# Kernel tuning notes

Measured on AMD Instinct MI355X. Metric: run time of the kernel, lower is better.

The kernel has to match this reference:

```python
import jax, jax.numpy as jnp
import numpy as np

NUM_HEADS = 16
D_MODEL = 1024


def setup_inputs() -> dict:
    key = jax.random.key(0)
    k1, k2, k3 = jax.random.split(key, 3)
    x = jax.random.normal(k1, (4, 2048, D_MODEL), dtype=jnp.float32)
    # torch.nn.Linear weights are [out_features, in_features]
    w_qkv = jax.random.normal(k2, (3 * D_MODEL, D_MODEL), dtype=jnp.float32) * (1.0 / np.sqrt(D_MODEL))
    w_o = jax.random.normal(k3, (D_MODEL, D_MODEL), dtype=jnp.float32) * (1.0 / np.sqrt(D_MODEL))
    return {"x": x, "w_qkv": w_qkv, "w_o": w_o}


def reference(x, w_qkv, w_o):
    b, n, _ = x.shape
    h = NUM_HEADS
    dh = D_MODEL // h  # head dim
    qkv = jnp.einsum('bnd,ed->bne', x, w_qkv)            # (b, n, 3*d_model)
    # Faithful to: rearrange(qkv, 'b n (h d) -> b h n d', h=h) then chunk(3, dim=-1)
    qkv = qkv.reshape(b, n, h, 3 * dh).transpose(0, 2, 1, 3)  # (b, h, n, 3*dh)
    q, k, v = jnp.split(qkv, 3, axis=-1)                 # each (b, h, n, dh)
    scale = 1.0 / jnp.sqrt(jnp.asarray(dh, dtype=x.dtype))
    scores = jnp.einsum('bhqd,bhkd->bhqk', q, k) * scale  # (b, h, n, n)
    attn = jax.nn.softmax(scores, axis=-1)
    out = jnp.einsum('bhqk,bhkd->bhqd', attn, v)          # (b, h, n, dh)
    out = out.transpose(0, 2, 1, 3).reshape(b, n, h * dh)  # 'b h n d -> b n (h d)'
    return jnp.einsum('bnd,ed->bne', out, w_o)
```

## Files before the change

kernel.cpp:

```cpp
#include <hip/hip_runtime.h>

#define BATCH 4
#define SEQ 2048
#define DM 1024
#define NH 16
#define DH 64
#define M_TOT (BATCH * SEQ)
#define EQKV (3 * DM)
#define QSCALE 0.18033688011112042f

typedef __bf16 bf16x8 __attribute__((ext_vector_type(8)));
typedef unsigned short u16x8 __attribute__((ext_vector_type(8)));
typedef float f32x2 __attribute__((ext_vector_type(2)));
typedef float f32x4 __attribute__((ext_vector_type(4)));
typedef float f32x16 __attribute__((ext_vector_type(16)));

static __device__ __forceinline__ unsigned short f2bf(float f) {
    unsigned int u = __builtin_bit_cast(unsigned int, f);
    u += 0x7fffu + ((u >> 16) & 1u);
    return (unsigned short)(u >> 16);
}

static __device__ __forceinline__ unsigned short f2bf_fast(float f) {
    return (unsigned short)((__builtin_bit_cast(unsigned int, f) + 0x8000u) >> 16);
}

static __device__ __forceinline__ unsigned int cvt_pk_bf16(float lo, float hi) {
    unsigned int r;
    asm("v_cvt_pk_bf16_f32 %0, %1, %2" : "=v"(r) : "v"(lo), "v"(hi));
    return r;
}

static __device__ __forceinline__ f32x2 pk_add(f32x2 a, f32x2 b) {
    f32x2 d;
    asm("v_pk_add_f32 %0, %1, %2" : "=v"(d) : "v"(a), "v"(b));
    return d;
}

static __device__ __forceinline__ float fast_exp2(float x) {
#if __has_builtin(__builtin_amdgcn_exp2f)
    return __builtin_amdgcn_exp2f(x);
#else
    return exp2f(x);
#endif
}

static __device__ __forceinline__ bf16x8 ld_frag(const ushort* p) {
    return *(const bf16x8*)p;
}

static __device__ __forceinline__ bf16x8 mk_frag(unsigned int a, unsigned int b,
                                                 unsigned int c, unsigned int d) {
    union { unsigned int u[4]; bf16x8 v; } t;
    t.u[0] = a; t.u[1] = b; t.u[2] = c; t.u[3] = d;
    return t.v;
}

static __device__ __forceinline__ void gload_lds16(const ushort* g, ushort* l) {
    __builtin_amdgcn_global_load_lds(
        (const __attribute__((address_space(1))) unsigned int*)g,
        (__attribute__((address_space(3))) unsigned int*)l,
        16, 0, 0);
}

__global__ __launch_bounds__(256) void detect_kernel(const ushort* __restrict__ x,
                                                     int* __restrict__ flag) {
    __shared__ int cnt[256];
    const int tid = threadIdx.x;
    int c = 0;
    for (int j = 0; j < 16; ++j) {
        unsigned short w = x[tid * 16 + j];
        int e = (w >> 7) & 0xFF;
        bool sane = (e == 0) || (e >= 0x60 && e <= 0x8F);
        c += sane ? 0 : 1;
    }
    cnt[tid] = c;
    __syncthreads();
    for (int s = 128; s > 0; s >>= 1) {
        if (tid < s) cnt[tid] += cnt[tid + s];
        __syncthreads();
    }
    if (tid == 0) flag[0] = (cnt[0] > 256) ? 1 : 0;
}

__global__ __launch_bounds__(256) void convert_frag_kernel(
    const void* __restrict__ src, ushort* __restrict__ dst, int R,
    const int* __restrict__ flag)
{
    const int t = blockIdx.x * 256 + threadIdx.x;
    if (t >= R * 128) return;
    const int m = t >> 7, kc = t & 127;

    u16x8 v;
    if (flag[0]) {
        const float* s = (const float*)src + (size_t)t * 8;
        #pragma unroll
        for (int j = 0; j < 8; ++j) v[j] = f2bf(s[j]);
    } else {
        v = *((const u16x8*)src + t);
    }
    const size_t o = (((size_t)(m >> 4) * 32 + (kc >> 2)) * 64 + (kc & 3) * 16 + (m & 15)) * 8;
    *(u16x8*)(dst + o) = v;
}

__global__ __launch_bounds__(256) void qkv_gemm_kernel(
    const ushort* __restrict__ XF, const ushort* __restrict__ WF,
    ushort* __restrict__ QF, ushort* __restrict__ KF, ushort* __restrict__ VF)
{
    const int lane = threadIdx.x & 63;
    const int wave = threadIdx.x >> 6;
    const int col  = lane & 15;
    const int quad = lane >> 4;
    const int orig = blockIdx.y * 24 + blockIdx.x;
    const int sid  = (orig & 7) * 192 + (orig >> 3);
    const int bx = sid % 24;
    const int by = sid / 24;
    const int m0 = by * 128 + (wave >> 1) * 64;
    const int e0 = bx * 128 + (wave & 1) * 64;
    const int mt0 = m0 >> 4, et0 = e0 >> 4;

    f32x4 acc[4][4];
    #pragma unroll
    for (int i = 0; i < 4; ++i)
        #pragma unroll
        for (int j = 0; j < 4; ++j) acc[i][j] = f32x4{0.f, 0.f, 0.f, 0.f};

    for (int kt = 0; kt < 32; ++kt) {
        bf16x8 a[4], b[4];
        #pragma unroll
        for (int i = 0; i < 4; ++i) {
            a[i] = ld_frag(XF + ((size_t)((mt0 + i) * 32 + kt) * 64 + lane) * 8);
            b[i] = ld_frag(WF + ((size_t)((et0 + i) * 32 + kt) * 64 + lane) * 8);
        }
        #pragma unroll
        for (int i = 0; i < 4; ++i)
            #pragma unroll
            for (int j = 0; j < 4; ++j)
                acc[i][j] = __builtin_amdgcn_mfma_f32_16x16x32_bf16(a[i], b[j], acc[i][j], 0, 0, 0);
    }

    #pragma unroll
    for (int ej = 0; ej < 4; ++ej) {
        const int e = e0 + ej * 16 + col;
        const int h = e / 192;
        const int c = e - h * 192;
        #pragma unroll
        for (int mi = 0; mi < 4; ++mi) {
            #pragma unroll
            for (int r = 0; r < 4; ++r) {
                const int m = m0 + mi * 16 + quad * 4 + r;
                const int bh = (m >> 11) * NH + h;
                const int n = m & (SEQ - 1);
                const float val = acc[mi][ej][r];
                if (c < 64) {
                    const int d = c;
                    QF[(((size_t)(bh * 64 + (n >> 5)) * 4 + (d >> 4)) * 64
                        + ((d >> 3) & 1) * 32 + (n & 31)) * 8 + (d & 7)] = f2bf_fast(val * QSCALE);
                } else if (c < 128) {
                    const int d = c - 64;
                    KF[(((size_t)(bh * 64 + (n >> 5)) * 4 + (d >> 4)) * 64
                        + ((d >> 3) & 1) * 32 + (n & 31)) * 8 + (d & 7)] = f2bf_fast(val);
                } else {
                    const int d = c - 128;
                    const int r4 = n & 15;
                    const int s4 = (r4 & 3) | (((r4 >> 3) & 1) << 2) | (((r4 >> 2) & 1) << 3);
                    VF[((((size_t)(bh * 32 + (n >> 6)) * 2 + (d >> 5)) * 4 + ((n >> 4) & 3)) * 64
                        + (s4 >> 3) * 32 + (d & 31)) * 8 + (s4 & 7)] = f2bf_fast(val);
                }
            }
        }
    }
}

__global__ __launch_bounds__(256) void attn_kernel(
    const ushort* __restrict__ QF, const ushort* __restrict__ KF,
    const ushort* __restrict__ VF, ushort* __restrict__ AOF)
{
    __shared__ ushort kvs[2][16 * 512];

    const int lane = threadIdx.x & 63;
    const int wave = threadIdx.x >> 6;
    const int half = lane >> 5;
    const int l31  = lane & 31;

    const int i = blockIdx.x;
    const int xcd = i & 7;
    const int s = i >> 3;
    const int qc = s & 15;
    const int bh = ((s >> 4) << 3) | xcd;
    const int q0 = qc * 128 + wave * 32;

    const ushort* qfb = QF + ((size_t)(bh * 64 + (q0 >> 5)) * 4) * 512;
    bf16x8 bq[4];
    #pragma unroll
    for (int d4 = 0; d4 < 4; ++d4) bq[d4] = ld_frag(qfb + d4 * 512 + lane * 8);

    const ushort* kfb = KF + (size_t)bh * 131072;
    const ushort* vfb = VF + (size_t)bh * 131072;

    f32x2 lp0 = {0.f, 0.f}, lp1 = {0.f, 0.f}, lp2 = {0.f, 0.f}, lp3 = {0.f, 0.f};
    f32x16 acc0 = {}, acc1 = {};

#define STAGE(it_, b_) do { \
        const size_t tb_ = (size_t)(it_) * 4096; \
        _Pragma("unroll") \
        for (int j_ = 0; j_ < 4; ++j_) { \
            const int f_ = wave * 4 + j_; \
            const ushort* src_ = (f_ < 8 ? kfb + tb_ + f_ * 512 \
                                         : vfb + tb_ + (f_ - 8) * 512) + lane * 8; \
            gload_lds16(src_, &kvs[b_][f_ * 512]); \
        } \
    } while (0)

#define LACC(v) do { \
        lp0 = pk_add(lp0, __builtin_shufflevector(v, v, 0, 1));   \
        lp1 = pk_add(lp1, __builtin_shufflevector(v, v, 2, 3));   \
        lp2 = pk_add(lp2, __builtin_shufflevector(v, v, 4, 5));   \
        lp3 = pk_add(lp3, __builtin_shufflevector(v, v, 6, 7));   \
        lp0 = pk_add(lp0, __builtin_shufflevector(v, v, 8, 9));   \
        lp1 = pk_add(lp1, __builtin_shufflevector(v, v, 10, 11)); \
        lp2 = pk_add(lp2, __builtin_shufflevector(v, v, 12, 13)); \
        lp3 = pk_add(lp3, __builtin_shufflevector(v, v, 14, 15)); \
    } while (0)

    STAGE(0, 0);
    __syncthreads();

    for (int it = 0; it < 32; ++it) {
        const int cb = it & 1;
        if (it + 1 < 32) STAGE(it + 1, cb ^ 1);

        const ushort* kp = &kvs[cb][0];

        f32x16 st0 = {}, st1 = {};
        #pragma unroll
        for (int d4 = 0; d4 < 4; ++d4) {
            bf16x8 ka0 = ld_frag(kp + d4 * 512 + lane * 8);
            bf16x8 ka1 = ld_frag(kp + (4 + d4) * 512 + lane * 8);
            st0 = __builtin_amdgcn_mfma_f32_32x32x16_bf16(ka0, bq[d4], st0, 0, 0, 0);
            st1 = __builtin_amdgcn_mfma_f32_32x32x16_bf16(ka1, bq[d4], st1, 0, 0, 0);
        }

        bf16x8 va0[4], va1[4];
        #pragma unroll
        for (int f4 = 0; f4 < 4; ++f4) {
            va0[f4] = ld_frag(kp + (8 + f4) * 512 + lane * 8);
            va1[f4] = ld_frag(kp + (12 + f4) * 512 + lane * 8);
        }

        #pragma unroll
        for (int t = 0; t < 16; ++t) st0[t] = fast_exp2(st0[t]);
        #pragma unroll
        for (int t = 0; t < 16; ++t) st1[t] = fast_exp2(st1[t]);
        LACC(st0);
        LACC(st1);

        bf16x8 pf[4];
        pf[0] = mk_frag(cvt_pk_bf16(st0[0],  st0[1]),  cvt_pk_bf16(st0[2],  st0[3]),
                        cvt_pk_bf16(st0[4],  st0[5]),  cvt_pk_bf16(st0[6],  st0[7]));
        pf[1] = mk_frag(cvt_pk_bf16(st0[8],  st0[9]),  cvt_pk_bf16(st0[10], st0[11]),
                        cvt_pk_bf16(st0[12], st0[13]), cvt_pk_bf16(st0[14], st0[15]));
        pf[2] = mk_frag(cvt_pk_bf16(st1[0],  st1[1]),  cvt_pk_bf16(st1[2],  st1[3]),
                        cvt_pk_bf16(st1[4],  st1[5]),  cvt_pk_bf16(st1[6],  st1[7]));
        pf[3] = mk_frag(cvt_pk_bf16(st1[8],  st1[9]),  cvt_pk_bf16(st1[10], st1[11]),
                        cvt_pk_bf16(st1[12], st1[13]), cvt_pk_bf16(st1[14], st1[15]));

        #pragma unroll
        for (int f4 = 0; f4 < 4; ++f4) {
            acc0 = __builtin_amdgcn_mfma_f32_32x32x16_bf16(va0[f4], pf[f4], acc0, 0, 0, 0);
            acc1 = __builtin_amdgcn_mfma_f32_32x32x16_bf16(va1[f4], pf[f4], acc1, 0, 0, 0);
        }

        __syncthreads();
    }
#undef LACC
#undef STAGE

    f32x2 lt = pk_add(pk_add(lp0, lp1), pk_add(lp2, lp3));
    float l_i = lt[0] + lt[1];
    l_i += __shfl_xor(l_i, 32, 64);

    const int b = bh >> 4, h = bh & (NH - 1);
    const float inv = 1.f / l_i;
    const int n_g = b * SEQ + q0 + l31;
    #pragma unroll
    for (int r = 0; r < 16; ++r) {
        const int d = (r & 3) + 8 * (r >> 2) + 4 * half;
        #pragma unroll
        for (int p = 0; p < 2; ++p) {
            const int e = h * 64 + p * 32 + d;
            const float val = (p == 0 ? acc0[r] : acc1[r]) * inv;
            AOF[(((size_t)(n_g >> 4) * 32 + (e >> 5)) * 64
                 + ((e >> 3) & 3) * 16 + (n_g & 15)) * 8 + (e & 7)] = f2bf_fast(val);
        }
    }
}

__global__ __launch_bounds__(256) void out_gemm_kernel(
    const ushort* __restrict__ AOF, const ushort* __restrict__ WOF,
    void* __restrict__ out, const int* __restrict__ flag)
{
    const int lane = threadIdx.x & 63;
    const int wave = threadIdx.x >> 6;
    const int col  = lane & 15;
    const int quad = lane >> 4;
    const int orig = blockIdx.y * 8 + blockIdx.x;
    const int sid  = (orig & 7) * 64 + (orig >> 3);
    const int bx = sid & 7;
    const int by = sid >> 3;
    const int m0 = by * 128 + (wave >> 1) * 64;
    const int e0 = bx * 128 + (wave & 1) * 64;
    const int mt0 = m0 >> 4, et0 = e0 >> 4;
    const int f = flag[0];

    f32x4 acc[4][4];
    #pragma unroll
    for (int i = 0; i < 4; ++i)
        #pragma unroll
        for (int j = 0; j < 4; ++j) acc[i][j] = f32x4{0.f, 0.f, 0.f, 0.f};

    for (int kt = 0; kt < 32; ++kt) {
        bf16x8 a[4], b[4];
        #pragma unroll
        for (int i = 0; i < 4; ++i) {
            a[i] = ld_frag(AOF + ((size_t)((mt0 + i) * 32 + kt) * 64 + lane) * 8);
            b[i] = ld_frag(WOF + ((size_t)((et0 + i) * 32 + kt) * 64 + lane) * 8);
        }
        #pragma unroll
        for (int i = 0; i < 4; ++i)
            #pragma unroll
            for (int j = 0; j < 4; ++j)
                acc[i][j] = __builtin_amdgcn_mfma_f32_16x16x32_bf16(a[i], b[j], acc[i][j], 0, 0, 0);
    }

    if (f == 0) {
        ushort* o = (ushort*)out;
        #pragma unroll
        for (int mi = 0; mi < 4; ++mi)
            #pragma unroll
            for (int ej = 0; ej < 4; ++ej)
                #pragma unroll
                for (int r = 0; r < 4; ++r)
                    o[(size_t)(m0 + mi * 16 + quad * 4 + r) * DM + e0 + ej * 16 + col] = f2bf_fast(acc[mi][ej][r]);
    } else {
        float* o = (float*)out;
        #pragma unroll
        for (int mi = 0; mi < 4; ++mi)
            #pragma unroll
            for (int ej = 0; ej < 4; ++ej)
                #pragma unroll
                for (int r = 0; r < 4; ++r)
                    o[(size_t)(m0 + mi * 16 + quad * 4 + r) * DM + e0 + ej * 16 + col] = acc[mi][ej][r];
    }
}

extern "C" void kernel_launch(void* const* d_in, const int* in_sizes, int n_in,
                              void* d_out, int out_size, void* d_ws, size_t ws_size,
                              hipStream_t stream) {
    const void* x_raw     = d_in[0];
    const void* w_qkv_raw = d_in[1];
    const void* w_o_raw   = d_in[2];

    char* ws = (char*)d_ws;
    int*    flag  = (int*)ws;
    ushort* XF    = (ushort*)(ws + 256);
    ushort* WQKVF = (ushort*)(ws + 256 + (16u << 20));
    ushort* WOF   = (ushort*)(ws + 256 + (22u << 20));
    ushort* QF    = (ushort*)(ws + 256 + (24u << 20));
    ushort* KF    = (ushort*)(ws + 256 + (40u << 20));
    ushort* VF    = (ushort*)(ws + 256 + (56u << 20));
    ushort* AOF   = XF;

    detect_kernel<<<1, 256, 0, stream>>>((const ushort*)x_raw, flag);
    convert_frag_kernel<<<M_TOT / 2, 256, 0, stream>>>(x_raw, XF, M_TOT, flag);
    convert_frag_kernel<<<EQKV / 2, 256, 0, stream>>>(w_qkv_raw, WQKVF, EQKV, flag);
    convert_frag_kernel<<<DM / 2, 256, 0, stream>>>(w_o_raw, WOF, DM, flag);

    qkv_gemm_kernel<<<dim3(EQKV / 128, M_TOT / 128), 256, 0, stream>>>(XF, WQKVF, QF, KF, VF);
    attn_kernel<<<dim3(BATCH * NH * (SEQ / 128)), 256, 0, stream>>>(QF, KF, VF, AOF);
    out_gemm_kernel<<<dim3(DM / 128, M_TOT / 128), 256, 0, stream>>>(AOF, WOF, d_out, flag);
}
```

Measured before the change: 301.8 us.

## Stage GEMM operand tiles through double-buffered LDS with async global-to-LDS loads

The QKV and output projection GEMMs now cooperatively copy each k-step's A and B fragment tiles into a double-buffered shared-memory area using direct global-to-LDS loads, prefetching step k+1 while computing step k. Waves then read fragments from LDS instead of each wave loading its own fragments from global memory. This removes redundant global loads, since pairs of waves previously fetched the same A or B tiles, and overlaps memory latency with MFMA work. The cost is a block-wide barrier every k-step and 32 KB of LDS per block, which may reduce occupancy. It also depends on a gload_lds16 helper, presumably defined in the hidden part of the file.

```diff
diff --git a/kernel.cpp b/kernel.cpp
--- a/kernel.cpp
+++ b/kernel.cpp
@@ -107,6 +107,9 @@
     const ushort* __restrict__ XF, const ushort* __restrict__ WF,
     ushort* __restrict__ QF, ushort* __restrict__ KF, ushort* __restrict__ VF)
 {
+    __shared__ ushort As[2][8 * 512];
+    __shared__ ushort Bs[2][8 * 512];
+
     const int lane = threadIdx.x & 63;
     const int wave = threadIdx.x >> 6;
     const int col  = lane & 15;
@@ -117,7 +120,9 @@
     const int by = sid / 24;
     const int m0 = by * 128 + (wave >> 1) * 64;
     const int e0 = bx * 128 + (wave & 1) * 64;
-    const int mt0 = m0 >> 4, et0 = e0 >> 4;
+    const int mt0 = by * 8, et0 = bx * 8;
+    const int wa = (wave >> 1) * 4;
+    const int wb = (wave & 1) * 4;
 
     f32x4 acc[4][4];
     #pragma unroll
@@ -125,19 +130,39 @@
         #pragma unroll
         for (int j = 0; j < 4; ++j) acc[i][j] = f32x4{0.f, 0.f, 0.f, 0.f};
 
+#define GSTAGE(kt_, b_) do { \
+        _Pragma("unroll") \
+        for (int j_ = 0; j_ < 2; ++j_) { \
+            const int c_ = wave * 2 + j_; \
+            gload_lds16(XF + (size_t)((mt0 + c_) * 32 + (kt_)) * 512 + lane * 8, \
+                        &As[b_][c_ * 512]); \
+            gload_lds16(WF + (size_t)((et0 + c_) * 32 + (kt_)) * 512 + lane * 8, \
+                        &Bs[b_][c_ * 512]); \
+        } \
+    } while (0)
+
+    GSTAGE(0, 0);
+    __syncthreads();
+
     for (int kt = 0; kt < 32; ++kt) {
+        const int cb = kt & 1;
+        if (kt + 1 < 32) GSTAGE(kt + 1, cb ^ 1);
+
         bf16x8 a[4], b[4];
         #pragma unroll
         for (int i = 0; i < 4; ++i) {
-            a[i] = ld_frag(XF + ((size_t)((mt0 + i) * 32 + kt) * 64 + lane) * 8);
-            b[i] = ld_frag(WF + ((size_t)((et0 + i) * 32 + kt) * 64 + lane) * 8);
+            a[i] = ld_frag(&As[cb][(wa + i) * 512] + lane * 8);
+            b[i] = ld_frag(&Bs[cb][(wb + i) * 512] + lane * 8);
         }
         #pragma unroll
         for (int i = 0; i < 4; ++i)
             #pragma unroll
             for (int j = 0; j < 4; ++j)
                 acc[i][j] = __builtin_amdgcn_mfma_f32_16x16x32_bf16(a[i], b[j], acc[i][j], 0, 0, 0);
-    }
+
+        __syncthreads();
+    }
+#undef GSTAGE
 
     #pragma unroll
     for (int ej = 0; ej < 4; ++ej) {
@@ -300,6 +325,9 @@
     const ushort* __restrict__ AOF, const ushort* __restrict__ WOF,
     void* __restrict__ out, const int* __restrict__ flag)
 {
+    __shared__ ushort As[2][8 * 512];
+    __shared__ ushort Bs[2][8 * 512];
+
     const int lane = threadIdx.x & 63;
     const int wave = threadIdx.x >> 6;
     const int col  = lane & 15;
@@ -310,7 +338,9 @@
     const int by = sid >> 3;
     const int m0 = by * 128 + (wave >> 1) * 64;
     const int e0 = bx * 128 + (wave & 1) * 64;
-    const int mt0 = m0 >> 4, et0 = e0 >> 4;
+    const int mt0 = by * 8, et0 = bx * 8;
+    const int wa = (wave >> 1) * 4;
+    const int wb = (wave & 1) * 4;
     const int f = flag[0];
 
     f32x4 acc[4][4];
@@ -319,19 +349,39 @@
         #pragma unroll
         for (int j = 0; j < 4; ++j) acc[i][j] = f32x4{0.f, 0.f, 0.f, 0.f};
 
+#define GSTAGE(kt_, b_) do { \
+        _Pragma("unroll") \
+        for (int j_ = 0; j_ < 2; ++j_) { \
+            const int c_ = wave * 2 + j_; \
+            gload_lds16(AOF + (size_t)((mt0 + c_) * 32 + (kt_)) * 512 + lane * 8, \
+                        &As[b_][c_ * 512]); \
+            gload_lds16(WOF + (size_t)((et0 + c_) * 32 + (kt_)) * 512 + lane * 8, \
+                        &Bs[b_][c_ * 512]); \
+        } \
+    } while (0)
+
+    GSTAGE(0, 0);
+    __syncthreads();
+
     for (int kt = 0; kt < 32; ++kt) {
+        const int cb = kt & 1;
+        if (kt + 1 < 32) GSTAGE(kt + 1, cb ^ 1);
+
         bf16x8 a[4], b[4];
         #pragma unroll
         for (int i = 0; i < 4; ++i) {
-            a[i] = ld_frag(AOF + ((size_t)((mt0 + i) * 32 + kt) * 64 + lane) * 8);
-            b[i] = ld_frag(WOF + ((size_t)((et0 + i) * 32 + kt) * 64 + lane) * 8);
+            a[i] = ld_frag(&As[cb][(wa + i) * 512] + lane * 8);
+            b[i] = ld_frag(&Bs[cb][(wb + i) * 512] + lane * 8);
         }
         #pragma unroll
         for (int i = 0; i < 4; ++i)
             #pragma unroll
             for (int j = 0; j < 4; ++j)
                 acc[i][j] = __builtin_amdgcn_mfma_f32_16x16x32_bf16(a[i], b[j], acc[i][j], 0, 0, 0);
-    }
+
+        __syncthreads();
+    }
+#undef GSTAGE
 
     if (f == 0) {
         ushort* o = (ushort*)out;
```

Result: no change. 297.9 us (-1.3%).
